# Optimization experiments

Measured on AMD Instinct MI355X. Metric: run time of the kernel, lower is better.

Reference implementation:

```python
import jax, jax.numpy as jnp
import numpy as np

I, H, B, T = 5, 256, 4096, 256


def _lstm_layer(x, w_ih, w_hh, b_ih, b_hh):
    # x: [B, T, in]; precompute the input-side gate GEMM for all timesteps
    xg = jnp.einsum('bti,gi->btg', x, w_ih) + b_ih + b_hh  # [B, T, 4H]
    h0 = jnp.zeros((x.shape[0], H), x.dtype)
    c0 = jnp.zeros((x.shape[0], H), x.dtype)

    def step(carry, xg_t):
        h, c = carry
        g = xg_t + h @ w_hh.T                      # [B, 4H]
        i_g, f_g, g_g, o_g = jnp.split(g, 4, axis=-1)  # torch gate order i,f,g,o
        c = jax.nn.sigmoid(f_g) * c + jax.nn.sigmoid(i_g) * jnp.tanh(g_g)
        h = jax.nn.sigmoid(o_g) * jnp.tanh(c)
        return (h, c), h

    (_, _), hs = jax.lax.scan(step, (h0, c0), jnp.swapaxes(xg, 0, 1))  # hs: [T, B, H]
    return jnp.swapaxes(hs, 0, 1)  # [B, T, H]


def setup_inputs() -> dict:
    key = jax.random.key(0)
    ks = jax.random.split(key, 12)
    s = 1.0 / np.sqrt(H)
    u = lambda k, shape: jax.random.uniform(k, shape, jnp.float32, -s, s)
    return {
        'x': jax.random.normal(ks[0], (B, T, I), jnp.float32),
        'w_ih0': u(ks[1], (4 * H, I)),
        'w_hh0': u(ks[2], (4 * H, H)),
        'b_ih0': u(ks[3], (4 * H,)),
        'b_hh0': u(ks[4], (4 * H,)),
        'w_ih1': u(ks[5], (4 * H, H)),
        'w_hh1': u(ks[6], (4 * H, H)),
        'b_ih1': u(ks[7], (4 * H,)),
        'b_hh1': u(ks[8], (4 * H,)),
        'fc_w': u(ks[9], (1, H)),
        'fc_b': u(ks[10], (1,)),
    }


def reference(x, w_ih0, w_hh0, b_ih0, b_hh0, w_ih1, w_hh1, b_ih1, b_hh1, fc_w, fc_b):
    h1 = _lstm_layer(x, w_ih0, w_hh0, b_ih0, b_hh0)   # [B, T, H]
    # dropout between layers is identity in eval mode
    h2 = _lstm_layer(h1, w_ih1, w_hh1, b_ih1, b_hh1)  # [B, T, H]
    out = jnp.einsum('bth,oh->bto', h2, fc_w) + fc_b  # [B, T, 1]
    return out
```

## Files before the change

### kernel.cpp

```cpp
#include <hip/hip_runtime.h>

typedef unsigned short u16;
typedef _Float16 f16_t;
typedef f16_t f16x8 __attribute__((ext_vector_type(8)));
typedef float f32x4 __attribute__((ext_vector_type(4)));
typedef unsigned u32x4 __attribute__((ext_vector_type(4)));

#define T_STEPS 256
#define IN_DIM  5
#define NBLK    256

#define WS_BIAS 1638400
#define WS_FC   1646592
#define WS_GX   1654784
#define GXS     524288
#define WS_CNT  (WS_GX + 8388608)

__device__ __forceinline__ float sigf(float x)  { return 1.0f / (1.0f + __expf(-x)); }
__device__ __forceinline__ float tanh_f(float x){ return 1.0f - 2.0f / (__expf(2.0f * x) + 1.0f); }

__global__ void prep_kernel(const float* __restrict__ wih0, const float* __restrict__ whh0,
                            const float* __restrict__ wih1, const float* __restrict__ whh1,
                            const float* __restrict__ bih0, const float* __restrict__ bhh0,
                            const float* __restrict__ bih1, const float* __restrict__ bhh1,
                            const float* __restrict__ fcw,
                            u16* __restrict__ wsw, float* __restrict__ biases,
                            u16* __restrict__ wsfc, unsigned* __restrict__ cnt)
{
    int j = blockIdx.x * blockDim.x + threadIdx.x;
    if (j < 102400) {
        int slice = j / 3200;
        int rem   = j - slice * 3200;
        int f     = rem >> 6;
        int lane  = rem & 63;
        int sub = slice >> 2, wv = slice & 3;
        int lrow = lane & 15;
        int kp = (lane >> 4) * 8;
        int nt, ks; bool g0;
        if (f < 18) { g0 = true;  nt = f / 9;  ks = f - nt * 9; }
        else        { int ff = f - 18; g0 = false; nt = ff >> 4; ks = ff & 15; }
        int wr = (nt * 2 + (lrow >> 3)) * 256 + sub * 32 + wv * 8 + (lrow & 7);
        u16 tmp[8];
#pragma unroll
        for (int e = 0; e < 8; ++e) {
            int k = kp + e;
            float v;
            if (g0) {
                v = (ks < 8) ? whh0[wr * 256 + ks * 32 + k]
                             : (k < IN_DIM ? wih0[wr * IN_DIM + k] : 0.0f);
            } else {
                v = (ks < 8) ? wih1[wr * 256 + ks * 32 + k]
                             : whh1[wr * 256 + (ks - 8) * 32 + k];
            }
            tmp[e] = __builtin_bit_cast(u16, (f16_t)v);
        }
        *(uint4*)(wsw + (size_t)j * 8) = *(uint4*)tmp;
    } else if (j < 103424) {
        int i = j - 102400;
        biases[i] = bih0[i] + bhh0[i];
    } else if (j < 104448) {
        int i = j - 103424;
        biases[1024 + i] = bih1[i] + bhh1[i];
    } else if (j < 104960) {
        int q = j - 104448;
        int ks = q >> 6, lane = q & 63;
        u16 tmp[8];
#pragma unroll
        for (int e = 0; e < 8; ++e) {
            float v = ((lane & 15) == 0) ? fcw[ks * 32 + (lane >> 4) * 8 + e] : 0.0f;
            tmp[e] = __builtin_bit_cast(u16, (f16_t)v);
        }
        *(uint4*)(wsfc + (size_t)q * 8) = *(uint4*)tmp;
    } else if (j < 107008) {
        cnt[j - 104960] = 0u;
    }
}

__global__ __launch_bounds__(256, 1) void lstm_fused(
    const float* __restrict__ x, const u16* __restrict__ wsw,
    const float* __restrict__ biases, const u16* __restrict__ wsfc,
    const float* __restrict__ fcb_g, float* __restrict__ out,
    u16* __restrict__ gxbase, unsigned* __restrict__ cnt)
{
    extern __shared__ char smem[];
    char* h0A = smem;
    char* h1A = smem + 32768;
    char* xbA = smem + 65536;
    char* h0B = smem + 69632;
    char* h1B = smem + 102400;
    char* xbB = smem + 135168;

    const int tid  = threadIdx.x;
    const int wv   = tid >> 6;
    const int lane = tid & 63;
    const int lrow = lane & 15;
    const int lkg  = lane >> 4;
    const int hf   = lrow >> 3;
    const int cj   = lrow & 7;
    const int sub  = blockIdx.x >> 5;
    const int grp  = blockIdx.x & 31;
    const int r0   = grp * 128;
    const int aswz = (lrow & 7) << 4;
    const int xswz = (lrow & 3) << 4;

    f16x8 w0[2][9], w1[2][16], wfc[8];
    const u16* wbase = wsw + (size_t)(sub * 4 + wv) * 25600;
#pragma unroll
    for (int nt = 0; nt < 2; ++nt)
#pragma unroll
        for (int ks = 0; ks < 9; ++ks) {
            w0[nt][ks] = *(const f16x8*)(wbase + (nt * 9 + ks) * 512 + lane * 8);
            asm volatile("" : "+a"(w0[nt][ks]));
            __builtin_amdgcn_sched_barrier(0);
        }
#pragma unroll
    for (int nt = 0; nt < 2; ++nt)
#pragma unroll
        for (int ks = 0; ks < 16; ++ks) {
            w1[nt][ks] = *(const f16x8*)(wbase + (18 + nt * 16 + ks) * 512 + lane * 8);
            asm volatile("" : "+a"(w1[nt][ks]));
            __builtin_amdgcn_sched_barrier(0);
        }
#pragma unroll
    for (int ks = 0; ks < 8; ++ks) {
        wfc[ks] = *(const f16x8*)(wsfc + ks * 512 + lane * 8);
        asm volatile("" : "+a"(wfc[ks]));
        __builtin_amdgcn_sched_barrier(0);
    }

    float b0[2], b1[2];
#pragma unroll
    for (int nt = 0; nt < 2; ++nt) {
        int wr = (nt * 2 + hf) * 256 + sub * 32 + wv * 8 + cj;
        b0[nt] = biases[wr];
        b1[nt] = biases[1024 + wr];
    }
    const float fcb = fcb_g[0];

    unsigned* fA    = cnt + grp * 8;
    unsigned* fB    = cnt + 256 + grp * 8;
    unsigned* fAme  = fA + sub;
    unsigned* fBme  = fB + sub;

    auto gxr = [&](int stream, int which, int parity) -> u16* {
        return gxbase + (size_t)((stream * 2 + which) * 2 + parity) * GXS + grp * 16384;
    };

    for (int i = tid; i < 139264 / 4; i += 256) ((unsigned*)smem)[i] = 0u;
    __syncthreads();
    {
        int i0 = tid, i1 = tid + 256;
        if (i0 < 320) { int row = i0 / 5, k = i0 - row * 5;
            float v = x[((size_t)(r0 + row) * T_STEPS + 0) * IN_DIM + k];
            *(u16*)(xbA + row * 64 + ((2 * k) ^ ((row & 3) << 4))) = __builtin_bit_cast(u16, (f16_t)v); }
        if (i1 < 320) { int row = i1 / 5, k = i1 - row * 5;
            float v = x[((size_t)(r0 + row) * T_STEPS + 0) * IN_DIM + k];
            *(u16*)(xbA + row * 64 + ((2 * k) ^ ((row & 3) << 4))) = __builtin_bit_cast(u16, (f16_t)v); }
    }
    __syncthreads();

    float c0A[4][2] = {}, c1A[4][2] = {}, c0B[4][2] = {}, c1B[4][2] = {};

    auto PUB = [&](u16* gxw, int mt, unsigned hv) {
        unsigned sh = __shfl_xor(hv, 1);
        const int rsel = cj & 1;
        unsigned w01;
        if (rsel) w01 = (sh >> 16) | (hv & 0xffff0000u);
        else      w01 = (hv & 0xffffu) | (sh << 16);
        unsigned p2 = __shfl_xor(w01, 2);
        unsigned lo4, hi4;
        if (cj & 2) { lo4 = p2;  hi4 = w01; }
        else        { lo4 = w01; hi4 = p2;  }
        unsigned q0 = __shfl_xor(lo4, 4), q1 = __shfl_xor(hi4, 4);
        u32x4 full;
        if (cj & 4) { full[0] = q0;  full[1] = q1;  full[2] = lo4; full[3] = hi4; }
        else        { full[0] = lo4; full[1] = hi4; full[2] = q0;  full[3] = q1;  }
        if (cj < 2) {
            int row = mt * 16 + lkg * 4 + hf * 2 + rsel;
            char* ap = (char*)gxw + sub * 4096 + row * 64 + wv * 16;
            asm volatile("global_store_dwordx4 %0, %1, off sc0 sc1"
                         :: "v"(ap), "v"(full) : "memory");
        }
    };

    auto GEMM0x = [&](const char* h0s, const char* xbs, float (&cs)[4][2], u16* gxw) {
#pragma unroll
        for (int mt = 0; mt < 4; ++mt) {
            f32x4 a0 = {}, a1 = {};
            const int arow = mt * 16 + lrow;
#pragma unroll
            for (int ks = 0; ks < 8; ++ks) {
                f16x8 a = *(const f16x8*)(h0s + arow * 512 + ((ks * 64 + lkg * 16) ^ aswz));
                a0 = __builtin_amdgcn_mfma_f32_16x16x32_f16(a, w0[0][ks], a0, 0, 0, 0);
                a1 = __builtin_amdgcn_mfma_f32_16x16x32_f16(a, w0[1][ks], a1, 0, 0, 0);
            }
            {
                f16x8 a = *(const f16x8*)(xbs + arow * 64 + ((lkg * 16) ^ xswz));
                a0 = __builtin_amdgcn_mfma_f32_16x16x32_f16(a, w0[0][8], a0, 0, 0, 0);
                a1 = __builtin_amdgcn_mfma_f32_16x16x32_f16(a, w0[1][8], a1, 0, 0, 0);
            }
#pragma unroll
            for (int r = 0; r < 4; ++r) { a0[r] += b0[0]; a1[r] += b0[1]; }
            float sA0 = __shfl_xor(hf ? a0[0] : a0[2], 8);
            float sA1 = __shfl_xor(hf ? a0[1] : a0[3], 8);
            float sB0 = __shfl_xor(hf ? a1[0] : a1[2], 8);
            float sB1 = __shfl_xor(hf ? a1[1] : a1[3], 8);
            unsigned hv = 0;
#pragma unroll
            for (int rr = 0; rr < 2; ++rr) {
                float sa = rr ? sA1 : sA0, sb = rr ? sB1 : sB0;
                float ig = hf ? sa : a0[rr];
                float fg = hf ? a0[2 + rr] : sa;
                float gg = hf ? sb : a1[rr];
                float og = hf ? a1[2 + rr] : sb;
                float c  = sigf(fg) * cs[mt][rr] + sigf(ig) * tanh_f(gg);
                cs[mt][rr] = c;
                float h  = sigf(og) * tanh_f(c);
                hv |= (unsigned)__builtin_bit_cast(u16, (f16_t)h) << (16 * rr);
            }
            PUB(gxw, mt, hv);
        }
    };
    auto GEMM1x = [&](const char* h0s, const char* h1s, float (&cs)[4][2], u16* gxw) {
#pragma unroll
        for (int mt = 0; mt < 4; ++mt) {
            f32x4 a0 = {}, a1 = {};
            const int arow = mt * 16 + lrow;
#pragma unroll
            for (int ks = 0; ks < 8; ++ks) {
                f16x8 a = *(const f16x8*)(h0s + arow * 512 + ((ks * 64 + lkg * 16) ^ aswz));
                a0 = __builtin_amdgcn_mfma_f32_16x16x32_f16(a, w1[0][ks], a0, 0, 0, 0);
                a1 = __builtin_amdgcn_mfma_f32_16x16x32_f16(a, w1[1][ks], a1, 0, 0, 0);
            }
#pragma unroll
            for (int ks = 0; ks < 8; ++ks) {
                f16x8 a = *(const f16x8*)(h1s + arow * 512 + ((ks * 64 + lkg * 16) ^ aswz));
                a0 = __builtin_amdgcn_mfma_f32_16x16x32_f16(a, w1[0][8 + ks], a0, 0, 0, 0);
                a1 = __builtin_amdgcn_mfma_f32_16x16x32_f16(a, w1[1][8 + ks], a1, 0, 0, 0);
            }
#pragma unroll
            for (int r = 0; r < 4; ++r) { a0[r] += b1[0]; a1[r] += b1[1]; }
            float sA0 = __shfl_xor(hf ? a0[0] : a0[2], 8);
            float sA1 = __shfl_xor(hf ? a0[1] : a0[3], 8);
            float sB0 = __shfl_xor(hf ? a1[0] : a1[2], 8);
            float sB1 = __shfl_xor(hf ? a1[1] : a1[3], 8);
            unsigned hv = 0;
#pragma unroll
            for (int rr = 0; rr < 2; ++rr) {
                float sa = rr ? sA1 : sA0, sb = rr ? sB1 : sB0;
                float ig = hf ? sa : a0[rr];
                float fg = hf ? a0[2 + rr] : sa;
                float gg = hf ? sb : a1[rr];
                float og = hf ? a1[2 + rr] : sb;
                float c  = sigf(fg) * cs[mt][rr] + sigf(ig) * tanh_f(gg);
                cs[mt][rr] = c;
                float h  = sigf(og) * tanh_f(c);
                hv |= (unsigned)__builtin_bit_cast(u16, (f16_t)h) << (16 * rr);
            }
            PUB(gxw, mt, hv);
        }
    };
    auto RELF = [&](unsigned* fme, unsigned val) {
        if (tid == 0)
            asm volatile("global_store_dword %0, %1, off sc0 sc1"
                         :: "v"(fme), "v"(val) : "memory");
    };
    auto SPINF = [&](unsigned* f, unsigned tgt) {
        if (wv == 0) {
            while (true) {
                unsigned v = tgt;
                if (lane < 8)
                    asm volatile("global_load_dword %0, %1, off sc0 sc1\n\t"
                                 "s_waitcnt vmcnt(0)"
                                 : "=v"(v) : "v"(f + lane) : "memory");
                bool ok = (lane >= 8) || (v >= tgt);
                if (__all(ok)) break;
                __builtin_amdgcn_s_sleep(1);
            }
        }
        __syncthreads();
    };
    auto FILL2 = [&](char* d0, const u16* s0, bool e0,
                     char* d1, const u16* s1, bool e1) {
        u32x4 q0[8], q1[8];
        const int row = tid & 63;
        const int base = (tid >> 6) * 2;
#pragma unroll
        for (int ss = 0; ss < 2; ++ss) {
            int s2 = base + ss;
            if (e0) {
                const char* sp = (const char*)s0 + s2 * 4096 + row * 64;
#pragma unroll
                for (int j = 0; j < 4; ++j)
                    asm volatile("global_load_dwordx4 %0, %1, off sc0 sc1"
                                 : "=&v"(q0[ss * 4 + j]) : "v"(sp + j * 16));
            }
            if (e1) {
                const char* sp = (const char*)s1 + s2 * 4096 + row * 64;
#pragma unroll
                for (int j = 0; j < 4; ++j)
                    asm volatile("global_load_dwordx4 %0, %1, off sc0 sc1"
                                 : "=&v"(q1[ss * 4 + j]) : "v"(sp + j * 16));
            }
        }
        asm volatile("s_waitcnt vmcnt(0)" ::: "memory");
        __builtin_amdgcn_sched_barrier(0);
        const int sw = (row & 7) << 4;
#pragma unroll
        for (int ss = 0; ss < 2; ++ss) {
            int s2 = base + ss;
            if (e0) {
#pragma unroll
                for (int j = 0; j < 4; ++j)
                    *(u32x4*)(d0 + row * 512 + ((s2 * 64 + j * 16) ^ sw)) = q0[ss * 4 + j];
            }
            if (e1) {
#pragma unroll
                for (int j = 0; j < 4; ++j)
                    *(u32x4*)(d1 + row * 512 + ((s2 * 64 + j * 16) ^ sw)) = q1[ss * 4 + j];
            }
        }
    };
    auto XLOAD = [&](int strOff, int tt, float& v0, float& v1) {
        v0 = 0.f; v1 = 0.f;
        int i0 = tid, i1 = tid + 256;
        if (i0 < 320) { int row = i0 / 5, k = i0 - row * 5;
            v0 = x[((size_t)(r0 + strOff + row) * T_STEPS + tt) * IN_DIM + k]; }
        if (i1 < 320) { int row = i1 / 5, k = i1 - row * 5;
            v1 = x[((size_t)(r0 + strOff + row) * T_STEPS + tt) * IN_DIM + k]; }
    };
    auto XSTAGE = [&](char* xbs, float v0, float v1) {
        int i0 = tid, i1 = tid + 256;
        if (i0 < 320) { int row = i0 / 5, k = i0 - row * 5;
            *(u16*)(xbs + row * 64 + ((2 * k) ^ ((row & 3) << 4))) = __builtin_bit_cast(u16, (f16_t)v0); }
        if (i1 < 320) { int row = i1 / 5, k = i1 - row * 5;
            *(u16*)(xbs + row * 64 + ((2 * k) ^ ((row & 3) << 4))) = __builtin_bit_cast(u16, (f16_t)v1); }
    };
    auto FC = [&](const char* h1s, int strOff, int tIdx, bool mine, int sub4) {
        if (wv == 0 && mine) {
            f32x4 acc = {};
            const int arow = sub4 * 16 + lrow;
#pragma unroll
            for (int ks = 0; ks < 8; ++ks) {
                f16x8 a = *(const f16x8*)(h1s + arow * 512 + ((ks * 64 + lkg * 16) ^ aswz));
                acc = __builtin_amdgcn_mfma_f32_16x16x32_f16(a, wfc[ks], acc, 0, 0, 0);
            }
            if (lrow == 0) {
#pragma unroll
                for (int r = 0; r < 4; ++r)
                    out[(size_t)(r0 + strOff + sub4 * 16 + lkg * 4 + r) * T_STEPS + tIdx] = acc[r] + fcb;
            }
        }
    };

#pragma unroll 1
    for (int t = 0; t < T_STEPS; ++t) {
        const int pc = t & 1, pp = (t - 1) & 1;

        float xa0, xa1, xbv0, xbv1;
        if (t + 1 < T_STEPS) { XLOAD(0, t + 1, xa0, xa1); } else { xa0 = 0.f; xa1 = 0.f; }
        XLOAD(64, t, xbv0, xbv1);

        GEMM0x(h0A, xbA, c0A, gxr(0, 0, pc));
        if (t > 0) GEMM1x(h0A, h1A, c1A, gxr(0, 1, pp));
        __syncthreads();
        RELF(fAme, (unsigned)(t + 1));

        SPINF(fB, (unsigned)t);
        FILL2(h0B, gxr(1, 0, pp), t > 0,
              h1B, gxr(1, 1, pc), t > 1);
        XSTAGE(xbB, xbv0, xbv1);
        __syncthreads();
        if (t > 1) FC(h1B, 64, t - 2, sub >= 4, sub - 4);

        GEMM0x(h0B, xbB, c0B, gxr(1, 0, pc));
        if (t > 0) GEMM1x(h0B, h1B, c1B, gxr(1, 1, pp));
        __syncthreads();
        RELF(fBme, (unsigned)(t + 1));

        SPINF(fA, (unsigned)(t + 1));
        FILL2(h0A, gxr(0, 0, pc), true,
              h1A, gxr(0, 1, pp), t > 0);
        if (t + 1 < T_STEPS) XSTAGE(xbA, xa0, xa1);
        __syncthreads();
        if (t > 0) FC(h1A, 0, t - 1, sub < 4, sub);
    }

    GEMM1x(h0A, h1A, c1A, gxr(0, 1, 1));
    __syncthreads();
    RELF(fAme, 257u);
    SPINF(fB, 256u);
    FILL2(h0B, gxr(1, 0, 1), true,
          h1B, gxr(1, 1, 0), true);
    __syncthreads();
    FC(h1B, 64, 254, sub >= 4, sub - 4);
    GEMM1x(h0B, h1B, c1B, gxr(1, 1, 1));
    __syncthreads();
    RELF(fBme, 257u);
    SPINF(fA, 257u);
    FILL2(h1A, gxr(0, 1, 1), true, h1A, gxr(0, 1, 1), false);
    __syncthreads();
    FC(h1A, 0, 255, sub < 4, sub);
    SPINF(fB, 257u);
    FILL2(h1B, gxr(1, 1, 1), true, h1B, gxr(1, 1, 1), false);
    __syncthreads();
    FC(h1B, 64, 255, sub >= 4, sub - 4);
}

extern "C" void kernel_launch(void* const* d_in, const int* in_sizes, int n_in,
                              void* d_out, int out_size, void* d_ws, size_t ws_size,
                              hipStream_t stream)
{
    const float* x    = (const float*)d_in[0];
    const float* wih0 = (const float*)d_in[1];
    const float* whh0 = (const float*)d_in[2];
    const float* bih0 = (const float*)d_in[3];
    const float* bhh0 = (const float*)d_in[4];
    const float* wih1 = (const float*)d_in[5];
    const float* whh1 = (const float*)d_in[6];
    const float* bih1 = (const float*)d_in[7];
    const float* bhh1 = (const float*)d_in[8];
    const float* fcw  = (const float*)d_in[9];
    const float* fcb  = (const float*)d_in[10];

    u16* wsw      = (u16*)d_ws;
    float* biases = (float*)((char*)d_ws + WS_BIAS);
    u16* wsfc     = (u16*)((char*)d_ws + WS_FC);
    u16* gxbase   = (u16*)((char*)d_ws + WS_GX);
    unsigned* cnt = (unsigned*)((char*)d_ws + WS_CNT);

    prep_kernel<<<419, 256, 0, stream>>>(wih0, whh0, wih1, whh1,
                                         bih0, bhh0, bih1, bhh1, fcw,
                                         wsw, biases, wsfc, cnt);
    lstm_fused<<<NBLK, 256, 139264, stream>>>(x, wsw, biases, wsfc, fcb,
                                              (float*)d_out, gxbase, cnt);
}
```

Before: 4.899 ms.

## Replace two interleaved batch streams per block with two co-resident blocks per CU

Each block used to interleave two 64-row batch streams (A/B) so that one stream's GEMMs could overlap the other's cross-block spin-wait. The change gives each block a single 64-row stream and launches 512 blocks with launch_bounds(256,2), shrinking LDS to about 76KB so two blocks can share a CU, and lets the hardware interleave them. The FC weights move from registers to LDS to relieve register pressure. The risk is that all 512 blocks must be co-resident for the spin-wait synchronisation to avoid deadlock, that registers may spill with the tighter budget, and that the explicit software overlap is lost.

```diff
diff --git a/kernel.cpp b/kernel.cpp
--- a/kernel.cpp
+++ b/kernel.cpp
@@ -8,12 +8,12 @@
 
 #define T_STEPS 256
 #define IN_DIM  5
-#define NBLK    256
+#define NBLK    512
 
 #define WS_BIAS 1638400
 #define WS_FC   1646592
 #define WS_GX   1654784
-#define GXS     524288
+#define GXS2    1048576
 #define WS_CNT  (WS_GX + 8388608)
 
 __device__ __forceinline__ float sigf(float x)  { return 1.0f / (1.0f + __expf(-x)); }
@@ -76,19 +76,17 @@
     }
 }
 
-__global__ __launch_bounds__(256, 1) void lstm_fused(
+__global__ __launch_bounds__(256, 2) void lstm_fused(
     const float* __restrict__ x, const u16* __restrict__ wsw,
     const float* __restrict__ biases, const u16* __restrict__ wsfc,
     const float* __restrict__ fcb_g, float* __restrict__ out,
     u16* __restrict__ gxbase, unsigned* __restrict__ cnt)
 {
     extern __shared__ char smem[];
-    char* h0A = smem;
-    char* h1A = smem + 32768;
-    char* xbA = smem + 65536;
-    char* h0B = smem + 69632;
-    char* h1B = smem + 102400;
-    char* xbB = smem + 135168;
+    char* h0b  = smem;
+    char* h1b  = smem + 32768;
+    char* xbb  = smem + 65536;
+    char* wfcL = smem + 69632;
 
     const int tid  = threadIdx.x;
     const int wv   = tid >> 6;
@@ -97,13 +95,14 @@
     const int lkg  = lane >> 4;
     const int hf   = lrow >> 3;
     const int cj   = lrow & 7;
-    const int sub  = blockIdx.x >> 5;
-    const int grp  = blockIdx.x & 31;
-    const int r0   = grp * 128;
+    const int bi   = blockIdx.x;
+    const int grp  = (bi & 31) | ((bi >> 8) << 5);
+    const int sub  = (bi >> 5) & 7;
+    const int r0   = grp * 64;
     const int aswz = (lrow & 7) << 4;
     const int xswz = (lrow & 3) << 4;
 
-    f16x8 w0[2][9], w1[2][16], wfc[8];
+    f16x8 w0[2][9], w1[2][16];
     const u16* wbase = wsw + (size_t)(sub * 4 + wv) * 25600;
 #pragma unroll
     for (int nt = 0; nt < 2; ++nt)
@@ -121,12 +120,6 @@
             asm volatile("" : "+a"(w1[nt][ks]));
             __builtin_amdgcn_sched_barrier(0);
         }
-#pragma unroll
-    for (int ks = 0; ks < 8; ++ks) {
-        wfc[ks] = *(const f16x8*)(wsfc + ks * 512 + lane * 8);
-        asm volatile("" : "+a"(wfc[ks]));
-        __builtin_amdgcn_sched_barrier(0);
-    }
 
     float b0[2], b1[2];
 #pragma unroll
@@ -137,29 +130,29 @@
     }
     const float fcb = fcb_g[0];
 
-    unsigned* fA    = cnt + grp * 8;
-    unsigned* fB    = cnt + 256 + grp * 8;
-    unsigned* fAme  = fA + sub;
-    unsigned* fBme  = fB + sub;
-
-    auto gxr = [&](int stream, int which, int parity) -> u16* {
-        return gxbase + (size_t)((stream * 2 + which) * 2 + parity) * GXS + grp * 16384;
-    };
-
-    for (int i = tid; i < 139264 / 4; i += 256) ((unsigned*)smem)[i] = 0u;
+    unsigned* f    = cnt + grp * 8;
+    unsigned* fme  = f + sub;
+
+    auto gxr = [&](int which, int parity) -> u16* {
+        return gxbase + (size_t)(which * 2 + parity) * GXS2 + grp * 16384;
+    };
+
+    for (int i = tid; i < 77824 / 4; i += 256) ((unsigned*)smem)[i] = 0u;
     __syncthreads();
+    for (int i = tid; i < 512; i += 256)
+        *(uint4*)(wfcL + i * 16) = *(const uint4*)(wsfc + (size_t)i * 8);
     {
         int i0 = tid, i1 = tid + 256;
         if (i0 < 320) { int row = i0 / 5, k = i0 - row * 5;
             float v = x[((size_t)(r0 + row) * T_STEPS + 0) * IN_DIM + k];
-            *(u16*)(xbA + row * 64 + ((2 * k) ^ ((row & 3) << 4))) = __builtin_bit_cast(u16, (f16_t)v); }
+            *(u16*)(xbb + row * 64 + ((2 * k) ^ ((row & 3) << 4))) = __builtin_bit_cast(u16, (f16_t)v); }
         if (i1 < 320) { int row = i1 / 5, k = i1 - row * 5;
             float v = x[((size_t)(r0 + row) * T_STEPS + 0) * IN_DIM + k];
-            *(u16*)(xbA + row * 64 + ((2 * k) ^ ((row & 3) << 4))) = __builtin_bit_cast(u16, (f16_t)v); }
+            *(u16*)(xbb + row * 64 + ((2 * k) ^ ((row & 3) << 4))) = __builtin_bit_cast(u16, (f16_t)v); }
     }
     __syncthreads();
 
-    float c0A[4][2] = {}, c1A[4][2] = {}, c0B[4][2] = {}, c1B[4][2] = {};
+    float c0[4][2] = {}, c1[4][2] = {};
 
     auto PUB = [&](u16* gxw, int mt, unsigned hv) {
         unsigned sh = __shfl_xor(hv, 1);
@@ -183,19 +176,19 @@
         }
     };
 
-    auto GEMM0x = [&](const char* h0s, const char* xbs, float (&cs)[4][2], u16* gxw) {
+    auto GEMM0x = [&](float (&cs)[4][2], u16* gxw) {
 #pragma unroll
         for (int mt = 0; mt < 4; ++mt) {
             f32x4 a0 = {}, a1 = {};
             const int arow = mt * 16 + lrow;
 #pragma unroll
             for (int ks = 0; ks < 8; ++ks) {
-                f16x8 a = *(const f16x8*)(h0s + arow * 512 + ((ks * 64 + lkg * 16) ^ aswz));
+                f16x8 a = *(const f16x8*)(h0b + arow * 512 + ((ks * 64 + lkg * 16) ^ aswz));
                 a0 = __builtin_amdgcn_mfma_f32_16x16x32_f16(a, w0[0][ks], a0, 0, 0, 0);
                 a1 = __builtin_amdgcn_mfma_f32_16x16x32_f16(a, w0[1][ks], a1, 0, 0, 0);
             }
             {
-                f16x8 a = *(const f16x8*)(xbs + arow * 64 + ((lkg * 16) ^ xswz));
+                f16x8 a = *(const f16x8*)(xbb + arow * 64 + ((lkg * 16) ^ xswz));
                 a0 = __builtin_amdgcn_mfma_f32_16x16x32_f16(a, w0[0][8], a0, 0, 0, 0);
                 a1 = __builtin_amdgcn_mfma_f32_16x16x32_f16(a, w0[1][8], a1, 0, 0, 0);
             }
@@ -221,20 +214,20 @@
             PUB(gxw, mt, hv);
         }
     };
-    auto GEMM1x = [&](const char* h0s, const char* h1s, float (&cs)[4][2], u16* gxw) {
+    auto GEMM1x = [&](float (&cs)[4][2], u16* gxw) {
 #pragma unroll
         for (int mt = 0; mt < 4; ++mt) {
             f32x4 a0 = {}, a1 = {};
             const int arow = mt * 16 + lrow;
 #pragma unroll
             for (int ks = 0; ks < 8; ++ks) {
-                f16x8 a = *(const f16x8*)(h0s + arow * 512 + ((ks * 64 + lkg * 16) ^ aswz));
+                f16x8 a = *(const f16x8*)(h0b + arow * 512 + ((ks * 64 + lkg * 16) ^ aswz));
                 a0 = __builtin_amdgcn_mfma_f32_16x16x32_f16(a, w1[0][ks], a0, 0, 0, 0);
                 a1 = __builtin_amdgcn_mfma_f32_16x16x32_f16(a, w1[1][ks], a1, 0, 0, 0);
             }
 #pragma unroll
             for (int ks = 0; ks < 8; ++ks) {
-                f16x8 a = *(const f16x8*)(h1s + arow * 512 + ((ks * 64 + lkg * 16) ^ aswz));
+                f16x8 a = *(const f16x8*)(h1b + arow * 512 + ((ks * 64 + lkg * 16) ^ aswz));
                 a0 = __builtin_amdgcn_mfma_f32_16x16x32_f16(a, w1[0][8 + ks], a0, 0, 0, 0);
                 a1 = __builtin_amdgcn_mfma_f32_16x16x32_f16(a, w1[1][8 + ks], a1, 0, 0, 0);
             }
@@ -260,12 +253,12 @@
             PUB(gxw, mt, hv);
         }
     };
-    auto RELF = [&](unsigned* fme, unsigned val) {
+    auto RELF = [&](unsigned val) {
         if (tid == 0)
             asm volatile("global_store_dword %0, %1, off sc0 sc1"
                          :: "v"(fme), "v"(val) : "memory");
     };
-    auto SPINF = [&](unsigned* f, unsigned tgt) {
+    auto SPINF = [&](unsigned tgt) {
         if (wv == 0) {
             while (true) {
                 unsigned v = tgt;
@@ -321,34 +314,35 @@
             }
         }
     };
-    auto XLOAD = [&](int strOff, int tt, float& v0, float& v1) {
+    auto XLOAD = [&](int tt, float& v0, float& v1) {
         v0 = 0.f; v1 = 0.f;
         int i0 = tid, i1 = tid + 256;
         if (i0 < 320) { int row = i0 / 5, k = i0 - row * 5;
-            v0 = x[((size_t)(r0 + strOff + row) * T_STEPS + tt) * IN_DIM + k]; }
+            v0 = x[((size_t)(r0 + row) * T_STEPS + tt) * IN_DIM + k]; }
         if (i1 < 320) { int row = i1 / 5, k = i1 - row * 5;
-            v1 = x[((size_t)(r0 + strOff + row) * T_STEPS + tt) * IN_DIM + k]; }
-    };
-    auto XSTAGE = [&](char* xbs, float v0, float v1) {
+            v1 = x[((size_t)(r0 + row) * T_STEPS + tt) * IN_DIM + k]; }
+    };
+    auto XSTAGE = [&](float v0, float v1) {
         int i0 = tid, i1 = tid + 256;
         if (i0 < 320) { int row = i0 / 5, k = i0 - row * 5;
-            *(u16*)(xbs + row * 64 + ((2 * k) ^ ((row & 3) << 4))) = __builtin_bit_cast(u16, (f16_t)v0); }
+            *(u16*)(xbb + row * 64 + ((2 * k) ^ ((row & 3) << 4))) = __builtin_bit_cast(u16, (f16_t)v0); }
         if (i1 < 320) { int row = i1 / 5, k = i1 - row * 5;
-            *(u16*)(xbs + row * 64 + ((2 * k) ^ ((row & 3) << 4))) = __builtin_bit_cast(u16, (f16_t)v1); }
-    };
-    auto FC = [&](const char* h1s, int strOff, int tIdx, bool mine, int sub4) {
-        if (wv == 0 && mine) {
+            *(u16*)(xbb + row * 64 + ((2 * k) ^ ((row & 3) << 4))) = __builtin_bit_cast(u16, (f16_t)v1); }
+    };
+    auto FC = [&](int tIdx) {
+        if (wv == 0 && sub < 4) {
             f32x4 acc = {};
-            const int arow = sub4 * 16 + lrow;
+            const int arow = sub * 16 + lrow;
 #pragma unroll
             for (int ks = 0; ks < 8; ++ks) {
-                f16x8 a = *(const f16x8*)(h1s + arow * 512 + ((ks * 64 + lkg * 16) ^ aswz));
-                acc = __builtin_amdgcn_mfma_f32_16x16x32_f16(a, wfc[ks], acc, 0, 0, 0);
+                f16x8 a  = *(const f16x8*)(h1b + arow * 512 + ((ks * 64 + lkg * 16) ^ aswz));
+                f16x8 wb = *(const f16x8*)(wfcL + ks * 1024 + lane * 16);
+                acc = __builtin_amdgcn_mfma_f32_16x16x32_f16(a, wb, acc, 0, 0, 0);
             }
             if (lrow == 0) {
 #pragma unroll
                 for (int r = 0; r < 4; ++r)
-                    out[(size_t)(r0 + strOff + sub4 * 16 + lkg * 4 + r) * T_STEPS + tIdx] = acc[r] + fcb;
+                    out[(size_t)(r0 + sub * 16 + lkg * 4 + r) * T_STEPS + tIdx] = acc[r] + fcb;
             }
         }
     };
@@ -357,54 +351,29 @@
     for (int t = 0; t < T_STEPS; ++t) {
         const int pc = t & 1, pp = (t - 1) & 1;
 
-        float xa0, xa1, xbv0, xbv1;
-        if (t + 1 < T_STEPS) { XLOAD(0, t + 1, xa0, xa1); } else { xa0 = 0.f; xa1 = 0.f; }
-        XLOAD(64, t, xbv0, xbv1);
-
-        GEMM0x(h0A, xbA, c0A, gxr(0, 0, pc));
-        if (t > 0) GEMM1x(h0A, h1A, c1A, gxr(0, 1, pp));
+        float xv0, xv1;
+        if (t + 1 < T_STEPS) { XLOAD(t + 1, xv0, xv1); } else { xv0 = 0.f; xv1 = 0.f; }
+
+        GEMM0x(c0, gxr(0, pc));
+        if (t > 0) GEMM1x(c1, gxr(1, pp));
         __syncthreads();
-        RELF(fAme, (unsigned)(t + 1));
-
-        SPINF(fB, (unsigned)t);
-        FILL2(h0B, gxr(1, 0, pp), t > 0,
-              h1B, gxr(1, 1, pc), t > 1);
-        XSTAGE(xbB, xbv0, xbv1);
+        RELF((unsigned)(t + 1));
+        if (t + 1 < T_STEPS) XSTAGE(xv0, xv1);
+
+        SPINF((unsigned)(t + 1));
+        FILL2(h0b, gxr(0, pc), true,
+              h1b, gxr(1, pp), t > 0);
         __syncthreads();
-        if (t > 1) FC(h1B, 64, t - 2, sub >= 4, sub - 4);
-
-        GEMM0x(h0B, xbB, c0B, gxr(1, 0, pc));
-        if (t > 0) GEMM1x(h0B, h1B, c1B, gxr(1, 1, pp));
-        __syncthreads();
-        RELF(fBme, (unsigned)(t + 1));
-
-        SPINF(fA, (unsigned)(t + 1));
-        FILL2(h0A, gxr(0, 0, pc), true,
-              h1A, gxr(0, 1, pp), t > 0);
-        if (t + 1 < T_STEPS) XSTAGE(xbA, xa0, xa1);
-        __syncthreads();
-        if (t > 0) FC(h1A, 0, t - 1, sub < 4, sub);
+        if (t > 0) FC(t - 1);
     }
 
-    GEMM1x(h0A, h1A, c1A, gxr(0, 1, 1));
+    GEMM1x(c1, gxr(1, 1));
     __syncthreads();
-    RELF(fAme, 257u);
-    SPINF(fB, 256u);
-    FILL2(h0B, gxr(1, 0, 1), true,
-          h1B, gxr(1, 1, 0), true);
+    RELF(257u);
+    SPINF(257u);
+    FILL2(h1b, gxr(1, 1), true, h1b, gxr(1, 1), false);
     __syncthreads();
-    FC(h1B, 64, 254, sub >= 4, sub - 4);
-    GEMM1x(h0B, h1B, c1B, gxr(1, 1, 1));
-    __syncthreads();
-    RELF(fBme, 257u);
-    SPINF(fA, 257u);
-    FILL2(h1A, gxr(0, 1, 1), true, h1A, gxr(0, 1, 1), false);
-    __syncthreads();
-    FC(h1A, 0, 255, sub < 4, sub);
-    SPINF(fB, 257u);
-    FILL2(h1B, gxr(1, 1, 1), true, h1B, gxr(1, 1, 1), false);
-    __syncthreads();
-    FC(h1B, 64, 255, sub >= 4, sub - 4);
+    FC(255);
 }
 
 extern "C" void kernel_launch(void* const* d_in, const int* in_sizes, int n_in,
@@ -432,6 +401,6 @@
     prep_kernel<<<419, 256, 0, stream>>>(wih0, whh0, wih1, whh1,
                                          bih0, bhh0, bih1, bhh1, fcw,
                                          wsw, biases, wsfc, cnt);
-    lstm_fused<<<NBLK, 256, 139264, stream>>>(x, wsw, biases, wsfc, fcb,
-                                              (float*)d_out, gxbase, cnt);
+    lstm_fused<<<NBLK, 256, 77824, stream>>>(x, wsw, biases, wsfc, fcb,
+                                             (float*)d_out, gxbase, cnt);
 }
```

After: 10.27 ms. 2.1x slower.
